# Kernel optimization log

Hardware: AMD Instinct MI355X
Metric: run time of the kernel (lower is better)

## Reference

```python
import jax, jax.numpy as jnp
import numpy as np

B, T, N, F_IN = 2, 4, 1024, 256
H, N_HIDDEN = 8, 128
SLOPE = 0.2
NEG_INF = -9e16


def setup_inputs() -> dict:
    key = jax.random.key(0)
    k1, k2, k3, k4 = jax.random.split(key, 4)
    h = jax.random.normal(k1, (B, T, N, F_IN), dtype=jnp.float32)
    adj_mat = jax.random.randint(k2, (N, N), 0, 2, dtype=jnp.int32)
    W = jax.random.normal(k3, (F_IN, H * N_HIDDEN), dtype=jnp.float32) * 0.05
    a = jax.random.normal(k4, (H, 2 * N_HIDDEN, 1), dtype=jnp.float32) * 0.05
    return {"h": h, "adj_mat": adj_mat, "W": W, "a": a}


def reference(h, adj_mat, W, a):
    b, t, n, _ = h.shape
    # linear transform: [B,T,N,F_in] @ [F_in, H*nh] -> [B,T,N,H*nh]
    ht = jnp.einsum('btjs,sh->btjh', h, W)
    # dropout is identity in eval mode
    ht = ht.reshape(b, t, n, H, N_HIDDEN).transpose(0, 1, 3, 2, 4)  # [B,T,H,N,nh]
    # additive attention scores
    a_src = a[:, :N_HIDDEN, :]   # [H, nh, 1]
    a_tgt = a[:, N_HIDDEN:, :]   # [H, nh, 1]
    src = jnp.einsum('bthnd,hdo->bthno', ht, a_src)  # [B,T,H,N,1]
    tgt = jnp.einsum('bthnd,hdo->bthno', ht, a_tgt)  # [B,T,H,N,1]
    e = src + jnp.swapaxes(tgt, -1, -2)              # [B,T,H,N,N]
    e = jnp.where(e >= 0, e, SLOPE * e)              # LeakyReLU
    e = jnp.where(adj_mat > 0, e, jnp.float32(NEG_INF))
    attention = jax.nn.softmax(e, axis=-1)
    # weighted aggregation: [B,T,H,N,N] @ [B,T,H,N,nh]
    h_prime = jnp.einsum('bthij,bthjd->bthid', attention, ht)
    # concat=False branch: mean over dim 0 (batch), as in the source
    return h_prime.mean(axis=0)  # [T,H,N,nh]
```

## Files before the change

kernel.cpp:

```cpp
#include <hip/hip_runtime.h>
#include <cstddef>
#include <cstdint>

#define B_ 2
#define T_ 4
#define N_ 1024
#define FIN_ 256
#define H_ 8
#define D_ 128
#define L2E_ 1.4426950408889634f

typedef __attribute__((ext_vector_type(8))) short short8;
typedef __attribute__((ext_vector_type(4))) float f32x4;

#define MFMA16(A, B, C) __builtin_amdgcn_mfma_f32_16x16x32_bf16((A), (B), (C), 0, 0, 0)

__device__ __forceinline__ unsigned short f2bf(float f) {
    uint32_t u = __float_as_uint(f);
    uint32_t r = (u + 0x7fffu + ((u >> 16) & 1u)) >> 16;
    return (unsigned short)r;
}

__device__ __forceinline__ uint32_t cvt_pk_bf16(float lo, float hi) {
    uint32_t r;
    asm volatile("v_cvt_pk_bf16_f32 %0, %1, %2" : "=v"(r) : "v"(lo), "v"(hi));
    return r;
}

__device__ __forceinline__ float fexp2(float x) {
#if __has_builtin(__builtin_amdgcn_exp2f)
    return __builtin_amdgcn_exp2f(x);
#else
    float r;
    asm("v_exp_f32 %0, %1" : "=v"(r) : "v"(x));
    return r;
#endif
}

__device__ __forceinline__ void load_lds16(const unsigned short* g, unsigned short* l) {
    __builtin_amdgcn_global_load_lds(
        (const __attribute__((address_space(1))) uint32_t*)g,
        (__attribute__((address_space(3))) uint32_t*)l, 16, 0, 0);
}

__global__ __launch_bounds__(256) void k_prep(const int* __restrict__ adj,
                                              const float* __restrict__ W,
                                              const float* __restrict__ a,
                                              unsigned short* __restrict__ Wt_bf,
                                              uint32_t* __restrict__ adjbits,
                                              float* __restrict__ wa) {
    __shared__ float wl[64][68];
    const int bid = blockIdx.x, tid = threadIdx.x;
    if (bid < 128) {
        const int w = bid * 256 + tid;
        const int i = w >> 5, jw = w & 31;
        const int4* p = (const int4*)(adj + (size_t)i * N_ + jw * 32);
        uint32_t bits = 0;
        #pragma unroll
        for (int q = 0; q < 8; ++q) {
            const int4 v = p[q];
            bits |= (uint32_t)(v.x > 0) << (q * 4 + 0);
            bits |= (uint32_t)(v.y > 0) << (q * 4 + 1);
            bits |= (uint32_t)(v.z > 0) << (q * 4 + 2);
            bits |= (uint32_t)(v.w > 0) << (q * 4 + 3);
        }
        adjbits[w] = bits;
    } else if (bid < 192) {
        const int tb  = bid - 128;
        const int hk0 = (tb >> 2) * 64;
        const int s0  = (tb & 3) * 64;
        {
            const int r  = tid >> 2;
            const int c0 = (tid & 3) * 16;
            #pragma unroll
            for (int k = 0; k < 4; ++k)
                *(float4*)&wl[r][c0 + k * 4] =
                    *(const float4*)(W + (size_t)(s0 + r) * (H_ * D_) + hk0 + c0 + k * 4);
        }
        __syncthreads();
        {
            const int r2 = tid >> 2;
            const int c2 = (tid & 3) * 16;
            unsigned short ob[16];
            #pragma unroll
            for (int k = 0; k < 16; ++k) ob[k] = f2bf(wl[c2 + k][r2]);
            unsigned short* dst = Wt_bf + (size_t)(hk0 + r2) * FIN_ + s0 + c2;
            *(uint4*)(dst)     = *(uint4*)&ob[0];
            *(uint4*)(dst + 8) = *(uint4*)&ob[8];
        }
    } else {
        const int o    = (bid - 192) * 256 + tid;
        const int head = o >> 9;
        const int st   = (o >> 8) & 1;
        const int s    = o & 255;
        const float* wr = W + (size_t)s * (H_ * D_) + head * D_;
        const float* ar = a + head * 256 + st * 128;
        float sum = 0.f;
        #pragma unroll
        for (int d = 0; d < 128; d += 4) {
            const float4 wv = *(const float4*)(wr + d);
            const float4 av = *(const float4*)(ar + d);
            sum += wv.x * av.x + wv.y * av.y + wv.z * av.z + wv.w * av.w;
        }
        wa[s * 16 + head * 2 + st] = sum;
    }
}

__global__ __launch_bounds__(256, 2) void k_gemm_sp(const float* __restrict__ h,
                                                    const unsigned short* __restrict__ Wt_bf,
                                                    const float* __restrict__ wa,
                                                    unsigned short* __restrict__ htT,
                                                    float* __restrict__ s1, float* __restrict__ s2,
                                                    float* __restrict__ t1, float* __restrict__ t2) {
    __shared__ __align__(16) char smem[24576];
    const int bid = blockIdx.x, tid = threadIdx.x;
    if (bid < 1024) {
        unsigned short* a_lds = (unsigned short*)smem;
        unsigned short* b_lds = (unsigned short*)(smem + 16384);
        const int xcd  = bid & 7;
        const int slot = bid >> 3;
        const int gid  = xcd * 8 + (slot >> 4);
        const int bt   = gid >> 3;
        const int n0   = (gid & 7) * 128;
        const int hk0  = (slot & 15) * 64;
        const int w = tid >> 6, lane = tid & 63;
        const int row16 = lane & 15, kgrp = lane >> 4;
        const int kswz = (kgrp ^ ((row16 >> 1) & 3)) * 8;
        const int ar  = tid >> 1;
        const int akh = tid & 1;
        const int asub = ar >> 4, arow = ar & 15;
        const int ax = (arow >> 1) & 3;
        const int aslot0 = ((akh * 2) ^ ax) * 8;
        const int aslot1 = ((akh * 2 + 1) ^ ax) * 8;
        const float* ga = h + ((size_t)bt * N_ + n0 + ar) * FIN_ + akh * 16;
        unsigned short* aw_ = a_lds + asub * 512 + arow * 32;
        const int brow = lane >> 2;
        const int bsb  = (lane & 3) ^ ((lane >> 3) & 3);
        const unsigned short* gb = Wt_bf + (size_t)(hk0 + w * 16 + brow) * FIN_ + bsb * 8;
        unsigned short* bw_ = b_lds + w * 512 + (size_t)lane * 8;

        float4 rf0, rf1, rf2, rf3;

#define LOADA(KS) {                                                            \
        const float* g = ga + (KS) * 32;                                       \
        rf0 = *(const float4*)(g);      rf1 = *(const float4*)(g + 4);         \
        rf2 = *(const float4*)(g + 8);  rf3 = *(const float4*)(g + 12); }

#define WRITEA(BUF) {                                                          \
        uint4 o0, o1;                                                          \
        o0.x = cvt_pk_bf16(rf0.x, rf0.y); o0.y = cvt_pk_bf16(rf0.z, rf0.w);    \
        o0.z = cvt_pk_bf16(rf1.x, rf1.y); o0.w = cvt_pk_bf16(rf1.z, rf1.w);    \
        o1.x = cvt_pk_bf16(rf2.x, rf2.y); o1.y = cvt_pk_bf16(rf2.z, rf2.w);    \
        o1.z = cvt_pk_bf16(rf3.x, rf3.y); o1.w = cvt_pk_bf16(rf3.z, rf3.w);    \
        unsigned short* ad = aw_ + (BUF) * 4096;                               \
        *(uint4*)(ad + aslot0) = o0;                                           \
        *(uint4*)(ad + aslot1) = o1; }

#define COMPK(BUF) {                                                           \
        const unsigned short* ab = a_lds + (BUF) * 4096;                       \
        const short8 bfv = *(const short8*)(b_lds + (BUF) * 2048 + w * 512 + row16 * 32 + kswz); \
        _Pragma("unroll")                                                      \
        for (int nt = 0; nt < 8; ++nt) {                                       \
            const short8 afv = *(const short8*)(ab + nt * 512 + row16 * 32 + kswz); \
            acc[nt] = MFMA16(afv, bfv, acc[nt]);                               \
        } }

        f32x4 acc[8];
        #pragma unroll
        for (int nt = 0; nt < 8; ++nt) acc[nt] = (f32x4){0.f, 0.f, 0.f, 0.f};

        LOADA(0)
        WRITEA(0)
        load_lds16(gb, bw_);
        LOADA(1)
        asm volatile("s_waitcnt vmcnt(4) lgkmcnt(0)" ::: "memory");
        __builtin_amdgcn_s_barrier();

        for (int ks = 0; ks < 8; ++ks) {
            const int cur = ks & 1;
            WRITEA(cur ^ 1)
            load_lds16(gb + ((ks + 1) & 7) * 32, bw_ + (cur ^ 1) * 2048);
            LOADA((ks + 2) & 7)
            COMPK(cur)
            asm volatile("s_waitcnt vmcnt(4) lgkmcnt(0)" ::: "memory");
            __builtin_amdgcn_s_barrier();
        }
#undef LOADA
#undef WRITEA
#undef COMPK
        const int hk   = hk0 + w * 16 + row16;
        const int head = hk >> 7;
        const int d    = hk & 127;
        unsigned short* ob = htT + ((size_t)(bt * H_ + head) * D_ + d) * N_;
        #pragma unroll
        for (int nt = 0; nt < 8; ++nt) {
            ushort4 v;
            v.x = f2bf(acc[nt][0]); v.y = f2bf(acc[nt][1]);
            v.z = f2bf(acc[nt][2]); v.w = f2bf(acc[nt][3]);
            *(ushort4*)(ob + n0 + nt * 16 + kgrp * 4) = v;
        }
    } else {
        float (*was)[16] = (float(*)[16])smem;
        {
            const int f = tid * 16;
            #pragma unroll
            for (int k = 0; k < 4; ++k)
                *(float4*)&was[f >> 4][k * 4] = *(const float4*)(wa + f + k * 4);
        }
        __syncthreads();
        const int r = tid >> 2, q = tid & 3;
        const int R = (bid - 1024) * 64 + r;
        const float* hrow = h + (size_t)R * FIN_ + q * 64;
        float acc[16];
        #pragma unroll
        for (int o = 0; o < 16; ++o) acc[o] = 0.f;
        for (int k = 0; k < 64; k += 4) {
            const float4 hv = *(const float4*)(hrow + k);
            const int s = q * 64 + k;
            #pragma unroll
            for (int kk = 0; kk < 4; ++kk) {
                const float hs = (kk == 0) ? hv.x : (kk == 1) ? hv.y : (kk == 2) ? hv.z : hv.w;
                #pragma unroll
                for (int o = 0; o < 16; ++o) acc[o] += hs * was[s + kk][o];
            }
        }
        #pragma unroll
        for (int o = 0; o < 16; ++o) {
            acc[o] += __shfl_xor(acc[o], 1);
            acc[o] += __shfl_xor(acc[o], 2);
        }
        const int bt = R >> 10, n = R & 1023;
        #pragma unroll
        for (int k = 0; k < 4; ++k) {
            const int o = q * 4 + k;
            const int head = o >> 1;
            const size_t idx = ((size_t)(bt * H_ + head)) * N_ + n;
            const float v = acc[o];
            if (o & 1) { t1[idx] = v * L2E_; t2[idx] = v * (0.2f * L2E_); }
            else       { s1[idx] = v * L2E_; s2[idx] = v * (0.2f * L2E_); }
        }
    }
}

struct SC {
    float4 a1l, a1h, a2l, a2h;
    uint32_t mA, mB;
};

__global__ __launch_bounds__(256, 2) void k_attn(const unsigned short* __restrict__ htT,
                                                 const float* __restrict__ s1,
                                                 const float* __restrict__ s2,
                                                 const float* __restrict__ t1,
                                                 const float* __restrict__ t2,
                                                 const uint32_t* __restrict__ adjbits,
                                                 float* __restrict__ out) {
    __shared__ __align__(16) char smem[65536];
    unsigned short* stg = (unsigned short*)smem;
    const int xcd  = blockIdx.x & 7;
    const int slot = blockIdx.x >> 3;
    const int th   = xcd * 4 + (slot >> 4);
    const int i0   = (slot & 15) * 64;
    const int tid = threadIdx.x;
    const int w = tid >> 6, lane = tid & 63;
    const int b = w & 1, isub = w >> 1;
    const int row16 = lane & 15, kgrp = lane >> 4, jrel = kgrp * 8;
    const int kswz = (kgrp ^ ((row16 >> 1) & 3)) * 8;
    const int bth = b * (T_ * H_) + th;
    const int iA  = i0 + isub * 32 + row16;
    const int iB  = iA + 16;
    const float s1A = s1[(size_t)bth * N_ + iA], s2A = s2[(size_t)bth * N_ + iA];
    const float s1B = s1[(size_t)bth * N_ + iB], s2B = s2[(size_t)bth * N_ + iB];
    const float* t1b = t1 + (size_t)bth * N_;
    const float* t2b = t2 + (size_t)bth * N_;
    const uint32_t* adjA = adjbits + (size_t)iA * (N_ / 32);
    const uint32_t* adjB = adjbits + (size_t)iB * (N_ / 32);

    const int sb  = w >> 1;
    const int sd0 = (w & 1) * 64 + (lane >> 2);
    const int sj  = ((lane & 3) ^ ((lane >> 3) & 3)) * 8;
    const unsigned short* gstg = htT + ((size_t)(sb * (T_ * H_) + th) * D_ + sd0) * N_ + sj;
    unsigned short* lstg = stg + (size_t)w * 2048 + (size_t)lane * 8;

#define STAGE(BUF, T32) {                                        \
        const unsigned short* gs = gstg + (size_t)(T32) * 32;    \
        unsigned short* ls = lstg + (BUF) * 8192;                \
        load_lds16(gs,           ls);                            \
        load_lds16(gs + 16 * N_, ls + 512);                      \
        load_lds16(gs + 32 * N_, ls + 1024);                     \
        load_lds16(gs + 48 * N_, ls + 1536); }

#define LOADSC(S, T32) {                                         \
        S.a1l = *(const float4*)(t1b + (T32) * 32 + jrel);       \
        S.a1h = *(const float4*)(t1b + (T32) * 32 + jrel + 4);   \
        S.a2l = *(const float4*)(t2b + (T32) * 32 + jrel);       \
        S.a2h = *(const float4*)(t2b + (T32) * 32 + jrel + 4);   \
        S.mA  = adjA[(T32)];                                     \
        S.mB  = adjB[(T32)]; }

    f32x4 accA[8], accB[8];
    #pragma unroll
    for (int nt = 0; nt < 8; ++nt) {
        accA[nt] = (f32x4){0.f, 0.f, 0.f, 0.f};
        accB[nt] = (f32x4){0.f, 0.f, 0.f, 0.f};
    }
    f32x4 daccA = (f32x4){0.f, 0.f, 0.f, 0.f};
    f32x4 daccB = (f32x4){0.f, 0.f, 0.f, 0.f};
    short8 ones8;
    {
        const short ov = (row16 == 0) ? (short)0x3F80 : (short)0;
        #pragma unroll
        for (int e = 0; e < 8; ++e) ones8[e] = ov;
    }
    const unsigned short* rdbase = stg + b * 4096 + row16 * 32 + kswz;

    SC scA, scB;

#define SUBP(BUFIDX, SCS, TNEXT)                                               \
    {                                                                          \
        const float tj1[8] = {SCS.a1l.x, SCS.a1l.y, SCS.a1l.z, SCS.a1l.w,      \
                              SCS.a1h.x, SCS.a1h.y, SCS.a1h.z, SCS.a1h.w};     \
        const float tj2[8] = {SCS.a2l.x, SCS.a2l.y, SCS.a2l.z, SCS.a2l.w,      \
                              SCS.a2h.x, SCS.a2h.y, SCS.a2h.z, SCS.a2h.w};     \
        const uint32_t mA = SCS.mA >> jrel;                                    \
        const uint32_t mB = SCS.mB >> jrel;                                    \
        float wvA[8], wvB[8];                                                  \
        _Pragma("unroll")                                                      \
        for (int e = 0; e < 8; ++e) {                                          \
            const float eA = fmaxf(s1A + tj1[e], s2A + tj2[e]);                \
            const float eB = fmaxf(s1B + tj1[e], s2B + tj2[e]);                \
            wvA[e] = ((mA >> e) & 1u) ? fexp2(eA) : 0.f;                       \
            wvB[e] = ((mB >> e) & 1u) ? fexp2(eB) : 0.f;                       \
        }                                                                      \
        short8 afA, afB;                                                       \
        _Pragma("unroll")                                                      \
        for (int p = 0; p < 4; ++p) {                                          \
            ((uint32_t*)&afA)[p] = cvt_pk_bf16(wvA[2 * p], wvA[2 * p + 1]);    \
            ((uint32_t*)&afB)[p] = cvt_pk_bf16(wvB[2 * p], wvB[2 * p + 1]);    \
        }                                                                      \
        LOADSC(SCS, (TNEXT))                                                   \
        const unsigned short* rb = rdbase + (BUFIDX) * 8192;                   \
        short8 bfr[8];                                                         \
        _Pragma("unroll")                                                      \
        for (int nt = 0; nt < 8; ++nt) bfr[nt] = *(const short8*)(rb + nt * 512); \
        _Pragma("unroll")                                                      \
        for (int nt = 0; nt < 8; ++nt) {                                       \
            accA[nt] = MFMA16(afA, bfr[nt], accA[nt]);                         \
            accB[nt] = MFMA16(afB, bfr[nt], accB[nt]);                         \
        }                                                                      \
        daccA = MFMA16(afA, ones8, daccA);                                     \
        daccB = MFMA16(afB, ones8, daccB);                                     \
    }

    STAGE(0, 0)
    STAGE(1, 1)
    LOADSC(scA, 0)
    LOADSC(scB, 1)

    for (int T = 0; T < 16; ++T) {
        const int pair  = T & 1;
        const int npair = pair ^ 1;
        asm volatile("s_waitcnt vmcnt(12)" ::: "memory");
        __builtin_amdgcn_s_barrier();
        asm volatile("" ::: "memory");
        STAGE(npair * 2,     (2 * T + 2) & 31)
        STAGE(npair * 2 + 1, (2 * T + 3) & 31)
        SUBP(pair * 2,     scA, (2 * T + 2) & 31)
        SUBP(pair * 2 + 1, scB, (2 * T + 3) & 31)
    }
#undef SUBP
#undef LOADSC
#undef STAGE

    __syncthreads();

    float ivA[4], ivB[4];
    #pragma unroll
    for (int r = 0; r < 4; ++r) {
        ivA[r] = __shfl(1.0f / daccA[r], kgrp * 16);
        ivB[r] = __shfl(1.0f / daccB[r], kgrp * 16);
    }

    float* comb = (float*)smem;
    if (b == 1) {
        #pragma unroll
        for (int nt = 0; nt < 8; ++nt)
            #pragma unroll
            for (int r = 0; r < 4; ++r) {
                const int il = isub * 32 + kgrp * 4 + r;
                const int d  = nt * 16 + row16;
                comb[il * 128 + d]        = accA[nt][r] * ivA[r];
                comb[(il + 16) * 128 + d] = accB[nt][r] * ivB[r];
            }
    }
    __syncthreads();
    if (b == 0) {
        #pragma unroll
        for (int nt = 0; nt < 8; ++nt)
            #pragma unroll
            for (int r = 0; r < 4; ++r) {
                const int il = isub * 32 + kgrp * 4 + r;
                const int d  = nt * 16 + row16;
                out[((size_t)th * N_ + i0 + il) * D_ + d] =
                    0.5f * (accA[nt][r] * ivA[r] + comb[il * 128 + d]);
                out[((size_t)th * N_ + i0 + il + 16) * D_ + d] =
                    0.5f * (accB[nt][r] * ivB[r] + comb[(il + 16) * 128 + d]);
            }
    }
}

extern "C" void kernel_launch(void* const* d_in, const int* in_sizes, int n_in,
                              void* d_out, int out_size, void* d_ws, size_t ws_size,
                              hipStream_t stream) {
    const float* h   = (const float*)d_in[0];
    const int*   adj = (const int*)d_in[1];
    const float* W   = (const float*)d_in[2];
    const float* a   = (const float*)d_in[3];
    float* out = (float*)d_out;

    char* p = (char*)d_ws;
    unsigned short* htT = (unsigned short*)p;  p += (size_t)B_ * T_ * H_ * D_ * N_ * 2;
    float* s1 = (float*)p;                     p += (size_t)B_ * T_ * H_ * N_ * 4;
    float* s2 = (float*)p;                     p += (size_t)B_ * T_ * H_ * N_ * 4;
    float* t1 = (float*)p;                     p += (size_t)B_ * T_ * H_ * N_ * 4;
    float* t2 = (float*)p;                     p += (size_t)B_ * T_ * H_ * N_ * 4;
    uint32_t* adjbits = (uint32_t*)p;          p += (size_t)N_ * N_ / 32 * 4;
    unsigned short* Wt_bf = (unsigned short*)p;p += (size_t)(H_ * D_) * FIN_ * 2;
    float* wa = (float*)p;

    k_prep<<<dim3(208), dim3(256), 0, stream>>>(adj, W, a, Wt_bf, adjbits, wa);
    k_gemm_sp<<<dim3(1152), dim3(256), 0, stream>>>(h, Wt_bf, wa, htT, s1, s2, t1, t2);
    k_attn<<<dim3(512), dim3(256), 0, stream>>>(htT, s1, s2, t1, t2, adjbits, out);
}
```

Measured before the change: 77.13 us.

## Split attention key dimension across two wave groups with 512-thread blocks

Doubles the attention block to 512 threads. The extra four waves process the second half of the key (j) range in parallel, each half running 16 steps instead of 32. Each wave now stages one tile per iteration, and the softmax denominators and partial accumulators from the two j-halves are combined through shared memory before the batch mean is written. This raises the number of waves in flight to hide latency, at the cost of extra LDS reductions, more barriers and tighter register limits from launch_bounds(512,4).

```diff
diff --git a/kernel.cpp b/kernel.cpp
--- a/kernel.cpp
+++ b/kernel.cpp
@@ -247,7 +247,7 @@
     uint32_t mA, mB;
 };
 
-__global__ __launch_bounds__(256, 2) void k_attn(const unsigned short* __restrict__ htT,
+__global__ __launch_bounds__(512, 4) void k_attn(const unsigned short* __restrict__ htT,
                                                  const float* __restrict__ s1,
                                                  const float* __restrict__ s2,
                                                  const float* __restrict__ t1,
@@ -262,40 +262,41 @@
     const int i0   = (slot & 15) * 64;
     const int tid = threadIdx.x;
     const int w = tid >> 6, lane = tid & 63;
-    const int b = w & 1, isub = w >> 1;
+    const int b = w & 1, jh = (w >> 1) & 1, isub = w >> 2;
     const int row16 = lane & 15, kgrp = lane >> 4, jrel = kgrp * 8;
     const int kswz = (kgrp ^ ((row16 >> 1) & 3)) * 8;
     const int bth = b * (T_ * H_) + th;
     const int iA  = i0 + isub * 32 + row16;
-    const int iB  = iA + 16;
     const float s1A = s1[(size_t)bth * N_ + iA], s2A = s2[(size_t)bth * N_ + iA];
-    const float s1B = s1[(size_t)bth * N_ + iB], s2B = s2[(size_t)bth * N_ + iB];
+    const float s1B = s1[(size_t)bth * N_ + iA + 16], s2B = s2[(size_t)bth * N_ + iA + 16];
     const float* t1b = t1 + (size_t)bth * N_;
     const float* t2b = t2 + (size_t)bth * N_;
     const uint32_t* adjA = adjbits + (size_t)iA * (N_ / 32);
-    const uint32_t* adjB = adjbits + (size_t)iB * (N_ / 32);
-
-    const int sb  = w >> 1;
-    const int sd0 = (w & 1) * 64 + (lane >> 2);
+    const uint32_t* adjB = adjbits + (size_t)(iA + 16) * (N_ / 32);
+
+    const int sq  = w & 3;
+    const int sg  = w >> 2;
+    const int ssb = sq >> 1;
+    const int sd0 = (sq & 1) * 64 + (lane >> 2);
     const int sj  = ((lane & 3) ^ ((lane >> 3) & 3)) * 8;
-    const unsigned short* gstg = htT + ((size_t)(sb * (T_ * H_) + th) * D_ + sd0) * N_ + sj;
-    unsigned short* lstg = stg + (size_t)w * 2048 + (size_t)lane * 8;
-
-#define STAGE(BUF, T32) {                                        \
-        const unsigned short* gs = gstg + (size_t)(T32) * 32;    \
-        unsigned short* ls = lstg + (BUF) * 8192;                \
+    const unsigned short* gstg = htT + ((size_t)(ssb * (T_ * H_) + th) * D_ + sd0) * N_ + sj;
+    unsigned short* lstg = stg + (size_t)sq * 2048 + (size_t)lane * 8;
+
+#define STAGE(BIDX, TS) {                                        \
+        const unsigned short* gs = gstg + (size_t)(TS) * 32;     \
+        unsigned short* ls = lstg + (BIDX) * 8192;               \
         load_lds16(gs,           ls);                            \
         load_lds16(gs + 16 * N_, ls + 512);                      \
         load_lds16(gs + 32 * N_, ls + 1024);                     \
         load_lds16(gs + 48 * N_, ls + 1536); }
 
-#define LOADSC(S, T32) {                                         \
-        S.a1l = *(const float4*)(t1b + (T32) * 32 + jrel);       \
-        S.a1h = *(const float4*)(t1b + (T32) * 32 + jrel + 4);   \
-        S.a2l = *(const float4*)(t2b + (T32) * 32 + jrel);       \
-        S.a2h = *(const float4*)(t2b + (T32) * 32 + jrel + 4);   \
-        S.mA  = adjA[(T32)];                                     \
-        S.mB  = adjB[(T32)]; }
+#define LOADSC(S, TS) {                                          \
+        S.a1l = *(const float4*)(t1b + (TS) * 32 + jrel);        \
+        S.a1h = *(const float4*)(t1b + (TS) * 32 + jrel + 4);    \
+        S.a2l = *(const float4*)(t2b + (TS) * 32 + jrel);        \
+        S.a2h = *(const float4*)(t2b + (TS) * 32 + jrel + 4);    \
+        S.mA  = adjA[(TS)];                                      \
+        S.mB  = adjB[(TS)]; }
 
     f32x4 accA[8], accB[8];
     #pragma unroll
@@ -313,16 +314,16 @@
     }
     const unsigned short* rdbase = stg + b * 4096 + row16 * 32 + kswz;
 
-    SC scA, scB;
-
-#define SUBP(BUFIDX, SCS, TNEXT)                                               \
+    SC sc;
+
+#define SUBP(BUFIDX, TNEXT)                                                    \
     {                                                                          \
-        const float tj1[8] = {SCS.a1l.x, SCS.a1l.y, SCS.a1l.z, SCS.a1l.w,      \
-                              SCS.a1h.x, SCS.a1h.y, SCS.a1h.z, SCS.a1h.w};     \
-        const float tj2[8] = {SCS.a2l.x, SCS.a2l.y, SCS.a2l.z, SCS.a2l.w,      \
-                              SCS.a2h.x, SCS.a2h.y, SCS.a2h.z, SCS.a2h.w};     \
-        const uint32_t mA = SCS.mA >> jrel;                                    \
-        const uint32_t mB = SCS.mB >> jrel;                                    \
+        const float tj1[8] = {sc.a1l.x, sc.a1l.y, sc.a1l.z, sc.a1l.w,          \
+                              sc.a1h.x, sc.a1h.y, sc.a1h.z, sc.a1h.w};         \
+        const float tj2[8] = {sc.a2l.x, sc.a2l.y, sc.a2l.z, sc.a2l.w,          \
+                              sc.a2h.x, sc.a2h.y, sc.a2h.z, sc.a2h.w};         \
+        const uint32_t mA = sc.mA >> jrel;                                     \
+        const uint32_t mB = sc.mB >> jrel;                                     \
         float wvA[8], wvB[8];                                                  \
         _Pragma("unroll")                                                      \
         for (int e = 0; e < 8; ++e) {                                          \
@@ -337,7 +338,7 @@
             ((uint32_t*)&afA)[p] = cvt_pk_bf16(wvA[2 * p], wvA[2 * p + 1]);    \
             ((uint32_t*)&afB)[p] = cvt_pk_bf16(wvB[2 * p], wvB[2 * p + 1]);    \
         }                                                                      \
-        LOADSC(SCS, (TNEXT))                                                   \
+        LOADSC(sc, (TNEXT))                                                    \
         const unsigned short* rb = rdbase + (BUFIDX) * 8192;                   \
         short8 bfr[8];                                                         \
         _Pragma("unroll")                                                      \
@@ -351,21 +352,16 @@
         daccB = MFMA16(afB, ones8, daccB);                                     \
     }
 
-    STAGE(0, 0)
-    STAGE(1, 1)
-    LOADSC(scA, 0)
-    LOADSC(scB, 1)
-
+    STAGE(sg, sg * 16)
+    LOADSC(sc, jh * 16)
+
+    #pragma unroll 2
     for (int T = 0; T < 16; ++T) {
-        const int pair  = T & 1;
-        const int npair = pair ^ 1;
-        asm volatile("s_waitcnt vmcnt(12)" ::: "memory");
+        asm volatile("s_waitcnt vmcnt(6)" ::: "memory");
         __builtin_amdgcn_s_barrier();
         asm volatile("" ::: "memory");
-        STAGE(npair * 2,     (2 * T + 2) & 31)
-        STAGE(npair * 2 + 1, (2 * T + 3) & 31)
-        SUBP(pair * 2,     scA, (2 * T + 2) & 31)
-        SUBP(pair * 2 + 1, scB, (2 * T + 3) & 31)
+        STAGE((((T + 1) & 1) * 2 + sg), sg * 16 + ((T + 1) & 15))
+        SUBP((T & 1) * 2 + jh, jh * 16 + ((T + 1) & 15))
     }
 #undef SUBP
 #undef LOADSC
@@ -373,27 +369,64 @@
 
     __syncthreads();
 
+    float* dden = (float*)smem;
+    if ((lane & 15) == 0) {
+        const int rb0 = isub * 32 + kgrp * 4;
+        #pragma unroll
+        for (int r = 0; r < 4; ++r) {
+            dden[(jh * 2 + b) * 64 + rb0 + r]      = daccA[r];
+            dden[(jh * 2 + b) * 64 + rb0 + 16 + r] = daccB[r];
+        }
+    }
+    __syncthreads();
     float ivA[4], ivB[4];
     #pragma unroll
     for (int r = 0; r < 4; ++r) {
-        ivA[r] = __shfl(1.0f / daccA[r], kgrp * 16);
-        ivB[r] = __shfl(1.0f / daccB[r], kgrp * 16);
-    }
+        const int rowA = isub * 32 + kgrp * 4 + r;
+        ivA[r] = 1.0f / (dden[b * 64 + rowA]      + dden[(2 + b) * 64 + rowA]);
+        ivB[r] = 1.0f / (dden[b * 64 + rowA + 16] + dden[(2 + b) * 64 + rowA + 16]);
+    }
+    __syncthreads();
 
     float* comb = (float*)smem;
-    if (b == 1) {
+    if (jh == 1) {
         #pragma unroll
         for (int nt = 0; nt < 8; ++nt)
             #pragma unroll
             for (int r = 0; r < 4; ++r) {
                 const int il = isub * 32 + kgrp * 4 + r;
                 const int d  = nt * 16 + row16;
-                comb[il * 128 + d]        = accA[nt][r] * ivA[r];
-                comb[(il + 16) * 128 + d] = accB[nt][r] * ivB[r];
+                comb[(b * 64 + il) * 128 + d]        = accA[nt][r];
+                comb[(b * 64 + il + 16) * 128 + d]   = accB[nt][r];
             }
     }
     __syncthreads();
-    if (b == 0) {
+    float opA[8][4], opB[8][4];
+    if (jh == 0) {
+        #pragma unroll
+        for (int nt = 0; nt < 8; ++nt)
+            #pragma unroll
+            for (int r = 0; r < 4; ++r) {
+                const int il = isub * 32 + kgrp * 4 + r;
+                const int d  = nt * 16 + row16;
+                opA[nt][r] = (accA[nt][r] + comb[(b * 64 + il) * 128 + d]) * ivA[r];
+                opB[nt][r] = (accB[nt][r] + comb[(b * 64 + il + 16) * 128 + d]) * ivB[r];
+            }
+        if (b == 1) {
+            #pragma unroll
+            for (int nt = 0; nt < 8; ++nt)
+                #pragma unroll
+                for (int r = 0; r < 4; ++r) {
+                    const int il = isub * 32 + kgrp * 4 + r;
+                    const int d  = nt * 16 + row16;
+                    comb[(64 + il) * 128 + d]      = opA[nt][r];
+                    comb[(64 + il + 16) * 128 + d] = opB[nt][r];
+                }
+        }
+    }
+    __syncthreads();
+
+    if (jh == 0 && b == 0) {
         #pragma unroll
         for (int nt = 0; nt < 8; ++nt)
             #pragma unroll
@@ -401,9 +434,9 @@
                 const int il = isub * 32 + kgrp * 4 + r;
                 const int d  = nt * 16 + row16;
                 out[((size_t)th * N_ + i0 + il) * D_ + d] =
-                    0.5f * (accA[nt][r] * ivA[r] + comb[il * 128 + d]);
+                    0.5f * (opA[nt][r] + comb[(64 + il) * 128 + d]);
                 out[((size_t)th * N_ + i0 + il + 16) * D_ + d] =
-                    0.5f * (accB[nt][r] * ivB[r] + comb[(il + 16) * 128 + d]);
+                    0.5f * (opB[nt][r] + comb[(64 + il + 16) * 128 + d]);
             }
     }
 }
@@ -429,5 +462,5 @@
 
     k_prep<<<dim3(208), dim3(256), 0, stream>>>(adj, W, a, Wt_bf, adjbits, wa);
     k_gemm_sp<<<dim3(1152), dim3(256), 0, stream>>>(h, Wt_bf, wa, htT, s1, s2, t1, t2);
-    k_attn<<<dim3(512), dim3(256), 0, stream>>>(htT, s1, s2, t1, t2, adjbits, out);
-}
+    k_attn<<<dim3(512), dim3(512), 0, stream>>>(htT, s1, s2, t1, t2, adjbits, out);
+}
```

Result: slower. 101.8 us (+31.9%).

## Halve shared staging to double-buffer single tiles and raise occupancy to four blocks

Applied to the files above, without the earlier changes.

The attention kernel's LDS staging drops from four tile buffers (two pairs) to two, halving shared memory to 32KB. Launch bounds rise to four blocks per CU. The main loop now processes one 32-column tile per iteration with a single score-context register set, so the barrier and waitcnt counts change. The aim is more resident waves to hide latency, at the cost of a shallower prefetch and twice as many barriers per block.

```diff
diff --git a/kernel.cpp b/kernel.cpp
--- a/kernel.cpp
+++ b/kernel.cpp
@@ -247,14 +247,14 @@
     uint32_t mA, mB;
 };
 
-__global__ __launch_bounds__(256, 2) void k_attn(const unsigned short* __restrict__ htT,
+__global__ __launch_bounds__(256, 4) void k_attn(const unsigned short* __restrict__ htT,
                                                  const float* __restrict__ s1,
                                                  const float* __restrict__ s2,
                                                  const float* __restrict__ t1,
                                                  const float* __restrict__ t2,
                                                  const uint32_t* __restrict__ adjbits,
                                                  float* __restrict__ out) {
-    __shared__ __align__(16) char smem[65536];
+    __shared__ __align__(16) char smem[32768];
     unsigned short* stg = (unsigned short*)smem;
     const int xcd  = blockIdx.x & 7;
     const int slot = blockIdx.x >> 3;
@@ -313,16 +313,16 @@
     }
     const unsigned short* rdbase = stg + b * 4096 + row16 * 32 + kswz;
 
-    SC scA, scB;
-
-#define SUBP(BUFIDX, SCS, TNEXT)                                               \
+    SC sc;
+
+#define SUBP(BUFIDX, TNEXT)                                                    \
     {                                                                          \
-        const float tj1[8] = {SCS.a1l.x, SCS.a1l.y, SCS.a1l.z, SCS.a1l.w,      \
-                              SCS.a1h.x, SCS.a1h.y, SCS.a1h.z, SCS.a1h.w};     \
-        const float tj2[8] = {SCS.a2l.x, SCS.a2l.y, SCS.a2l.z, SCS.a2l.w,      \
-                              SCS.a2h.x, SCS.a2h.y, SCS.a2h.z, SCS.a2h.w};     \
-        const uint32_t mA = SCS.mA >> jrel;                                    \
-        const uint32_t mB = SCS.mB >> jrel;                                    \
+        const float tj1[8] = {sc.a1l.x, sc.a1l.y, sc.a1l.z, sc.a1l.w,          \
+                              sc.a1h.x, sc.a1h.y, sc.a1h.z, sc.a1h.w};         \
+        const float tj2[8] = {sc.a2l.x, sc.a2l.y, sc.a2l.z, sc.a2l.w,          \
+                              sc.a2h.x, sc.a2h.y, sc.a2h.z, sc.a2h.w};         \
+        const uint32_t mA = sc.mA >> jrel;                                     \
+        const uint32_t mB = sc.mB >> jrel;                                     \
         float wvA[8], wvB[8];                                                  \
         _Pragma("unroll")                                                      \
         for (int e = 0; e < 8; ++e) {                                          \
@@ -337,7 +337,7 @@
             ((uint32_t*)&afA)[p] = cvt_pk_bf16(wvA[2 * p], wvA[2 * p + 1]);    \
             ((uint32_t*)&afB)[p] = cvt_pk_bf16(wvB[2 * p], wvB[2 * p + 1]);    \
         }                                                                      \
-        LOADSC(SCS, (TNEXT))                                                   \
+        LOADSC(sc, (TNEXT))                                                    \
         const unsigned short* rb = rdbase + (BUFIDX) * 8192;                   \
         short8 bfr[8];                                                         \
         _Pragma("unroll")                                                      \
@@ -352,20 +352,14 @@
     }
 
     STAGE(0, 0)
-    STAGE(1, 1)
-    LOADSC(scA, 0)
-    LOADSC(scB, 1)
-
-    for (int T = 0; T < 16; ++T) {
-        const int pair  = T & 1;
-        const int npair = pair ^ 1;
-        asm volatile("s_waitcnt vmcnt(12)" ::: "memory");
+    LOADSC(sc, 0)
+
+    for (int t = 0; t < 32; ++t) {
+        asm volatile("s_waitcnt vmcnt(6) lgkmcnt(0)" ::: "memory");
         __builtin_amdgcn_s_barrier();
         asm volatile("" ::: "memory");
-        STAGE(npair * 2,     (2 * T + 2) & 31)
-        STAGE(npair * 2 + 1, (2 * T + 3) & 31)
-        SUBP(pair * 2,     scA, (2 * T + 2) & 31)
-        SUBP(pair * 2 + 1, scB, (2 * T + 3) & 31)
+        STAGE((t + 1) & 1, (t + 1) & 31)
+        SUBP(t & 1, (t + 1) & 31)
     }
 #undef SUBP
 #undef LOADSC
```

Result: slower. 91.91 us (+19.2%).

## Load MFMA B operands directly from global into registers, drop LDS staging

Applied to the files above, without the earlier changes.

Replaces the LDS double-buffered staging of htT tiles (global-to-LDS loads, barriers, swizzled LDS reads) with direct per-lane global loads of the B fragments into registers. The loads are software-pipelined across two register sets with vmcnt waits instead of block barriers. This removes LDS traffic and barriers and shrinks shared memory to the combine buffer only. In exchange, each of the two waves per batch that share a tile now fetches it redundantly from global/L2, register pressure rises from 16 extra short8 registers, and the loads are less coalesced.

```diff
diff --git a/kernel.cpp b/kernel.cpp
--- a/kernel.cpp
+++ b/kernel.cpp
@@ -254,8 +254,7 @@
                                                  const float* __restrict__ t2,
                                                  const uint32_t* __restrict__ adjbits,
                                                  float* __restrict__ out) {
-    __shared__ __align__(16) char smem[65536];
-    unsigned short* stg = (unsigned short*)smem;
+    __shared__ __align__(16) float comb[64 * 128];
     const int xcd  = blockIdx.x & 7;
     const int slot = blockIdx.x >> 3;
     const int th   = xcd * 4 + (slot >> 4);
@@ -264,7 +263,6 @@
     const int w = tid >> 6, lane = tid & 63;
     const int b = w & 1, isub = w >> 1;
     const int row16 = lane & 15, kgrp = lane >> 4, jrel = kgrp * 8;
-    const int kswz = (kgrp ^ ((row16 >> 1) & 3)) * 8;
     const int bth = b * (T_ * H_) + th;
     const int iA  = i0 + isub * 32 + row16;
     const int iB  = iA + 16;
@@ -274,20 +272,12 @@
     const float* t2b = t2 + (size_t)bth * N_;
     const uint32_t* adjA = adjbits + (size_t)iA * (N_ / 32);
     const uint32_t* adjB = adjbits + (size_t)iB * (N_ / 32);
-
-    const int sb  = w >> 1;
-    const int sd0 = (w & 1) * 64 + (lane >> 2);
-    const int sj  = ((lane & 3) ^ ((lane >> 3) & 3)) * 8;
-    const unsigned short* gstg = htT + ((size_t)(sb * (T_ * H_) + th) * D_ + sd0) * N_ + sj;
-    unsigned short* lstg = stg + (size_t)w * 2048 + (size_t)lane * 8;
-
-#define STAGE(BUF, T32) {                                        \
-        const unsigned short* gs = gstg + (size_t)(T32) * 32;    \
-        unsigned short* ls = lstg + (BUF) * 8192;                \
-        load_lds16(gs,           ls);                            \
-        load_lds16(gs + 16 * N_, ls + 512);                      \
-        load_lds16(gs + 32 * N_, ls + 1024);                     \
-        load_lds16(gs + 48 * N_, ls + 1536); }
+    const unsigned short* hfb = htT + ((size_t)bth * D_ + row16) * N_ + jrel;
+
+#define LOADBF(DST, T32) {                                                     \
+        _Pragma("unroll")                                                      \
+        for (int nt = 0; nt < 8; ++nt)                                         \
+            DST[nt] = *(const short8*)(hfb + (size_t)nt * 16 * N_ + (T32) * 32); }
 
 #define LOADSC(S, T32) {                                         \
         S.a1l = *(const float4*)(t1b + (T32) * 32 + jrel);       \
@@ -311,11 +301,11 @@
         #pragma unroll
         for (int e = 0; e < 8; ++e) ones8[e] = ov;
     }
-    const unsigned short* rdbase = stg + b * 4096 + row16 * 32 + kswz;
-
+
+    short8 bfX[8], bfY[8];
     SC scA, scB;
 
-#define SUBP(BUFIDX, SCS, TNEXT)                                               \
+#define SUBP(BF, SCS)                                                          \
     {                                                                          \
         const float tj1[8] = {SCS.a1l.x, SCS.a1l.y, SCS.a1l.z, SCS.a1l.w,      \
                               SCS.a1h.x, SCS.a1h.y, SCS.a1h.z, SCS.a1h.w};     \
@@ -337,41 +327,32 @@
             ((uint32_t*)&afA)[p] = cvt_pk_bf16(wvA[2 * p], wvA[2 * p + 1]);    \
             ((uint32_t*)&afB)[p] = cvt_pk_bf16(wvB[2 * p], wvB[2 * p + 1]);    \
         }                                                                      \
-        LOADSC(SCS, (TNEXT))                                                   \
-        const unsigned short* rb = rdbase + (BUFIDX) * 8192;                   \
-        short8 bfr[8];                                                         \
-        _Pragma("unroll")                                                      \
-        for (int nt = 0; nt < 8; ++nt) bfr[nt] = *(const short8*)(rb + nt * 512); \
         _Pragma("unroll")                                                      \
         for (int nt = 0; nt < 8; ++nt) {                                       \
-            accA[nt] = MFMA16(afA, bfr[nt], accA[nt]);                         \
-            accB[nt] = MFMA16(afB, bfr[nt], accB[nt]);                         \
+            accA[nt] = MFMA16(afA, BF[nt], accA[nt]);                          \
+            accB[nt] = MFMA16(afB, BF[nt], accB[nt]);                          \
         }                                                                      \
         daccA = MFMA16(afA, ones8, daccA);                                     \
         daccB = MFMA16(afB, ones8, daccB);                                     \
     }
 
-    STAGE(0, 0)
-    STAGE(1, 1)
+    LOADBF(bfX, 0)
     LOADSC(scA, 0)
-    LOADSC(scB, 1)
-
-    for (int T = 0; T < 16; ++T) {
-        const int pair  = T & 1;
-        const int npair = pair ^ 1;
-        asm volatile("s_waitcnt vmcnt(12)" ::: "memory");
-        __builtin_amdgcn_s_barrier();
-        asm volatile("" ::: "memory");
-        STAGE(npair * 2,     (2 * T + 2) & 31)
-        STAGE(npair * 2 + 1, (2 * T + 3) & 31)
-        SUBP(pair * 2,     scA, (2 * T + 2) & 31)
-        SUBP(pair * 2 + 1, scB, (2 * T + 3) & 31)
+
+    for (int tt = 0; tt < 16; ++tt) {
+        const int t0 = tt * 2;
+        LOADBF(bfY, t0 + 1)
+        LOADSC(scB, t0 + 1)
+        asm volatile("s_waitcnt vmcnt(14)" ::: "memory");
+        SUBP(bfX, scA)
+        LOADBF(bfX, (t0 + 2) & 31)
+        LOADSC(scA, (t0 + 2) & 31)
+        asm volatile("s_waitcnt vmcnt(14)" ::: "memory");
+        SUBP(bfY, scB)
     }
 #undef SUBP
 #undef LOADSC
-#undef STAGE
-
-    __syncthreads();
+#undef LOADBF
 
     float ivA[4], ivB[4];
     #pragma unroll
@@ -380,7 +361,6 @@
         ivB[r] = __shfl(1.0f / daccB[r], kgrp * 16);
     }
 
-    float* comb = (float*)smem;
     if (b == 1) {
         #pragma unroll
         for (int nt = 0; nt < 8; ++nt)
```

Result: slower. 118.9 us (+54.1%).
